# Optimization experiments

Measured on AMD Instinct MI355X. Metric: run time of the kernel, lower is better.

The kernel has to match this reference:

```python
import jax, jax.numpy as jnp
import numpy as np

N_NODES = 50000
E_TRAIN = 800000
E_POS = 200000
E_NEG = 200000
F_IN = 128


def gcn_conv(x, W, b, src, dst, n):
    """PyG-style GCNConv: add self-loops, symmetric deg^{-1/2} norm, linear, scatter-add."""
    loop = jnp.arange(n, dtype=src.dtype)
    s = jnp.concatenate([src, loop])  # [E+N]
    d = jnp.concatenate([dst, loop])
    deg = jax.ops.segment_sum(jnp.ones(d.shape, dtype=x.dtype), d, num_segments=n)
    dis = jax.lax.rsqrt(jnp.maximum(deg, 1.0))  # deg >= 1 due to self-loops
    norm = dis[s] * dis[d]  # [E+N]
    h = x @ W  # [N, out]
    msg = h[s] * norm[:, None]  # gather + per-edge scale
    return jax.ops.segment_sum(msg, d, num_segments=n) + b


def reference(x, train_pos_edge_index, pos_edge_index, neg_edge_index, W1, b1, W2, b2, W3, b3):
    src, dst = train_pos_edge_index[0], train_pos_edge_index[1]
    h = jax.nn.relu(gcn_conv(x, W1, b1, src, dst, N_NODES))
    h = jax.nn.relu(gcn_conv(h, W2, b2, src, dst, N_NODES))
    h = gcn_conv(h, W3, b3, src, dst, N_NODES)
    te = jnp.concatenate([pos_edge_index, neg_edge_index], axis=-1)  # [2, E_pos+E_neg]
    x_j = h[te[0]]
    x_i = h[te[1]]
    return jnp.einsum('ef,ef->e', x_i, x_j)


def setup_inputs() -> dict:
    key = jax.random.key(0)
    ks = jax.random.split(key, 10)
    glorot = lambda k, fi, fo: jax.random.normal(k, (fi, fo), dtype=jnp.float32) * np.float32(np.sqrt(2.0 / (fi + fo)))
    return {
        'x': jax.random.normal(ks[0], (N_NODES, F_IN), dtype=jnp.float32),
        'train_pos_edge_index': jax.random.randint(ks[1], (2, E_TRAIN), 0, N_NODES, dtype=jnp.int32),
        'pos_edge_index': jax.random.randint(ks[2], (2, E_POS), 0, N_NODES, dtype=jnp.int32),
        'neg_edge_index': jax.random.randint(ks[3], (2, E_NEG), 0, N_NODES, dtype=jnp.int32),
        'W1': glorot(ks[4], F_IN, 256), 'b1': jnp.zeros((256,), jnp.float32),
        'W2': glorot(ks[5], 256, 128), 'b2': jnp.zeros((128,), jnp.float32),
        'W3': glorot(ks[6], 128, 64), 'b3': jnp.zeros((64,), jnp.float32),
    }
```

## Files before the change

### kernel.cpp

```cpp
#include <hip/hip_runtime.h>
#include <math.h>

#define N_NODES 50000
#define E_TRAIN 800000
#define E_POS 200000
#define E_NEG 200000

#define NBUCK 196
#define BSTRIDE 5120


__device__ inline void split_bf16(float f, short& h, short& l) {
    unsigned u = __float_as_uint(f);
    h = (short)(u >> 16);
    float rem = f - __uint_as_float(u & 0xFFFF0000u);
    l = (short)(__float_as_uint(rem) >> 16);
}

__device__ inline unsigned short f2bf_rne(float f) {
    unsigned u = __float_as_uint(f);
    unsigned r = u + 0x7FFFu + ((u >> 16) & 1u);
    return (unsigned short)(r >> 16);
}

__device__ inline float bf2f(unsigned short h) {
    return __uint_as_float(((unsigned)h) << 16);
}


__global__ void partA_kernel(const int* __restrict__ src, const int* __restrict__ dst,
                             int* __restrict__ gcount, unsigned int* __restrict__ temp, int e) {
    __shared__ int hist[NBUCK];
    __shared__ int base[NBUCK];
    __shared__ int lcur[NBUCK];
    int tid = threadIdx.x;
    for (int i = tid; i < NBUCK; i += 256) hist[i] = 0;
    __syncthreads();
    int start = blockIdx.x * 4096;
    int stop = min(start + 4096, e);
    for (int i = start + tid; i < stop; i += 256)
        atomicAdd(&hist[dst[i] >> 8], 1);
    __syncthreads();
    for (int i = tid; i < NBUCK; i += 256) {
        base[i] = atomicAdd(&gcount[i], hist[i]);
        lcur[i] = 0;
    }
    __syncthreads();
    for (int i = start + tid; i < stop; i += 256) {
        int d = dst[i];
        int b = d >> 8;
        int off = atomicAdd(&lcur[b], 1);
        temp[(size_t)b * BSTRIDE + base[b] + off] = ((unsigned)src[i] << 8) | (unsigned)(d & 255);
    }
}

__global__ void scanb_kernel(const int* __restrict__ gcount, int* __restrict__ gbase) {
    __shared__ int s[256];
    int t = threadIdx.x;
    int v = (t < NBUCK) ? gcount[t] : 0;
    s[t] = v;
    __syncthreads();
    for (int d = 1; d < 256; d <<= 1) {
        int u = 0;
        if (t >= d) u = s[t - d];
        __syncthreads();
        if (t >= d) s[t] += u;
        __syncthreads();
    }
    if (t < NBUCK) gbase[t] = s[t] - v;
}


__global__ void partB_kernel(const unsigned int* __restrict__ temp,
                             const int* __restrict__ gcount, const int* __restrict__ gbase,
                             float* __restrict__ dis, int* __restrict__ offs, int* __restrict__ ends,
                             unsigned short* __restrict__ csr) {
    __shared__ int cnt[256];
    __shared__ int loc[256];
    __shared__ int cursor[256];
    int b = blockIdx.x;
    int t = threadIdx.x;
    int total = gcount[b];
    size_t tbase = (size_t)b * BSTRIDE;
    cnt[t] = 0;
    __syncthreads();
    for (int i = t; i < total; i += 256)
        atomicAdd(&cnt[temp[tbase + i] & 255], 1);
    __syncthreads();
    int c = cnt[t];
    loc[t] = c;
    __syncthreads();
    for (int d = 1; d < 256; d <<= 1) {
        int u = 0;
        if (t >= d) u = loc[t - d];
        __syncthreads();
        if (t >= d) loc[t] += u;
        __syncthreads();
    }
    int excl = loc[t] - c;
    int node = b * 256 + t;
    int gstart = gbase[b] + excl;
    if (node < N_NODES) {
        dis[node] = 1.0f / sqrtf((float)(c + 1));
        offs[node] = gstart;
        ends[node] = gstart + c;
    }
    cursor[t] = gstart;
    __syncthreads();
    for (int i = t; i < total; i += 256) {
        unsigned v = temp[tbase + i];
        int pos = atomicAdd(&cursor[v & 255], 1);
        csr[pos] = (unsigned short)(v >> 8);
    }
}

#define WTOT (128 * 256 + 256 * 128 + 128 * 64)

__global__ void prep_kernel(const float* __restrict__ W1, short* __restrict__ W1h, short* __restrict__ W1l,
                            const float* __restrict__ W2, short* __restrict__ W2h, short* __restrict__ W2l,
                            const float* __restrict__ W3, short* __restrict__ W3h, short* __restrict__ W3l,
                            const float* __restrict__ x, unsigned short* __restrict__ xb, int n4) {
    int i = blockIdx.x * blockDim.x + threadIdx.x;
    if (i < WTOT) {
        const float* W; short *Wh, *Wl; int K, N;
        if (i < 128 * 256) { W = W1; Wh = W1h; Wl = W1l; K = 128; N = 256; }
        else if (i < 128 * 256 + 256 * 128) { i -= 128 * 256; W = W2; Wh = W2h; Wl = W2l; K = 256; N = 128; }
        else { i -= 128 * 256 + 256 * 128; W = W3; Wh = W3h; Wl = W3l; K = 128; N = 64; }
        int k = i / N, n = i - k * N;
        short h, l;
        split_bf16(W[i], h, l);
        Wh[(size_t)n * K + k] = h;
        Wl[(size_t)n * K + k] = l;
    } else {
        int j = i - WTOT;
        if (j < n4) {
            float4 v = ((const float4*)x)[j];
            ushort4 o;
            o.x = f2bf_rne(v.x); o.y = f2bf_rne(v.y);
            o.z = f2bf_rne(v.z); o.w = f2bf_rne(v.w);
            ((ushort4*)xb)[j] = o;
        }
    }
}


typedef short bf16x8 __attribute__((ext_vector_type(8)));
typedef float f32x4 __attribute__((ext_vector_type(4)));

template<int BN, bool BR, bool OBF>
__global__ __launch_bounds__(512) void gemm_fulln_kernel(
        const float* __restrict__ A,
        const short* __restrict__ Bth, const short* __restrict__ Btl,
        const float* __restrict__ bias, float* __restrict__ C,
        unsigned short* __restrict__ Cb,
        int M, int K) {
    constexpr int NI = BN / 16;
    constexpr int BCH = BN * 4;
    constexpr int BP = (BCH + 511) / 512;
    constexpr size_t BSZ = (size_t)2 * BN * 40 * 2;
    constexpr size_t TSZ = (size_t)8 * 16 * 68 * 4;
    __shared__ __align__(16) char smem[BSZ > TSZ ? BSZ : TSZ];
    short* Bhi = (short*)smem;
    short* Blo = (short*)(smem + (size_t)BN * 40 * 2);
    float* tr  = (float*)smem;

    int tid = threadIdx.x;
    int lane = tid & 63;
    int wv = tid >> 6;
    int brow = blockIdx.x * 128;
    int m_lane = lane & 15;
    int kgrp = lane >> 4;

    int myrow = brow + wv * 16 + m_lane;
    if (myrow >= M) myrow = M - 1;
    const float* Ap = &A[(size_t)myrow * K + kgrp * 8];

    f32x4 acc[NI];
    #pragma unroll
    for (int i = 0; i < NI; i++) acc[i] = (f32x4){0.f, 0.f, 0.f, 0.f};

    int4 bhReg[BP], blReg[BP];
    float4 aN0, aN1, aC0, aC1;

    auto loadB = [&](int k0) {
        #pragma unroll
        for (int p = 0; p < BP; p++) {
            int idx = p * 512 + tid;
            if (idx < BCH) {
                int col = idx >> 2;
                int kc = idx & 3;
                size_t o = (size_t)col * K + k0 + kc * 8;
                bhReg[p] = *(const int4*)&Bth[o];
                blReg[p] = *(const int4*)&Btl[o];
            }
        }
    };
    auto loadA = [&](int k0) {
        aN0 = *(const float4*)&Ap[k0];
        aN1 = *(const float4*)&Ap[k0 + 4];
    };

    loadB(0); loadA(0);

    for (int k0 = 0; k0 < K; k0 += 32) {
        aC0 = aN0; aC1 = aN1;
        #pragma unroll
        for (int p = 0; p < BP; p++) {
            int idx = p * 512 + tid;
            if (idx < BCH) {
                int col = idx >> 2;
                int kc = idx & 3;
                *(int4*)&Bhi[col * 40 + kc * 8] = bhReg[p];
                *(int4*)&Blo[col * 40 + kc * 8] = blReg[p];
            }
        }
        __syncthreads();

        if (k0 + 32 < K) { loadB(k0 + 32); loadA(k0 + 32); }

        bf16x8 ah, al;
        {
            short h, l;
            split_bf16(aC0.x, h, l); ah[0] = h; al[0] = l;
            split_bf16(aC0.y, h, l); ah[1] = h; al[1] = l;
            split_bf16(aC0.z, h, l); ah[2] = h; al[2] = l;
            split_bf16(aC0.w, h, l); ah[3] = h; al[3] = l;
            split_bf16(aC1.x, h, l); ah[4] = h; al[4] = l;
            split_bf16(aC1.y, h, l); ah[5] = h; al[5] = l;
            split_bf16(aC1.z, h, l); ah[6] = h; al[6] = l;
            split_bf16(aC1.w, h, l); ah[7] = h; al[7] = l;
        }
        #pragma unroll
        for (int ni = 0; ni < NI; ni++) {
            int boff = (ni * 16 + m_lane) * 40 + kgrp * 8;
            bf16x8 bh = *(const bf16x8*)&Bhi[boff];
            bf16x8 bl = *(const bf16x8*)&Blo[boff];
            acc[ni] = __builtin_amdgcn_mfma_f32_16x16x32_bf16(ah, bh, acc[ni], 0, 0, 0);
            acc[ni] = __builtin_amdgcn_mfma_f32_16x16x32_bf16(al, bh, acc[ni], 0, 0, 0);
            acc[ni] = __builtin_amdgcn_mfma_f32_16x16x32_bf16(ah, bl, acc[ni], 0, 0, 0);
        }
        __syncthreads();
    }

    #pragma unroll
    for (int c = 0; c < NI / 4; c++) {
        #pragma unroll
        for (int q = 0; q < 4; q++) {
            int ni = c * 4 + q;
            float bb = 0.f;
            if (BR) bb = bias[ni * 16 + m_lane];
            #pragma unroll
            for (int reg = 0; reg < 4; reg++) {
                float v = acc[ni][reg];
                if (BR) v = fmaxf(v + bb, 0.f);
                tr[wv * 1088 + (kgrp * 4 + reg) * 68 + q * 16 + m_lane] = v;
            }
        }
        #pragma unroll
        for (int j = 0; j < 4; j++) {
            int r = (lane >> 4) + j * 4;
            int g = lane & 15;
            float4 v = *(const float4*)&tr[wv * 1088 + r * 68 + g * 4];
            int row = brow + wv * 16 + r;
            if (row < M) {
                if (OBF) {
                    ushort4 o;
                    o.x = f2bf_rne(v.x); o.y = f2bf_rne(v.y);
                    o.z = f2bf_rne(v.z); o.w = f2bf_rne(v.w);
                    *(ushort4*)&Cb[(size_t)row * BN + c * 64 + g * 4] = o;
                } else {
                    *(float4*)&C[(size_t)row * BN + c * 64 + g * 4] = v;
                }
            }
        }
    }
}


#define AGG_WAVES 12800
#define AGG_BLOCKS (AGG_WAVES / 4)

template<int F, bool RELU, bool BIAS>
__global__ void aggregate_bf16_kernel(const unsigned short* __restrict__ xb,
                                      float* __restrict__ out,
                                      const float* __restrict__ dis,
                                      const int* __restrict__ starts,
                                      const int* __restrict__ ends,
                                      const unsigned short* __restrict__ csr_src,
                                      const float* __restrict__ bias,
                                      int n) {
    int wid = (blockIdx.x * blockDim.x + threadIdx.x) >> 6;
    int lane = threadIdx.x & 63;
    constexpr int VPT = F / 64;

    for (int v = wid; v < n; v += AGG_WAVES) {
        float dv = dis[v];
        float acc[VPT];
        if constexpr (VPT == 2) {
            ushort2 sv = *(const ushort2*)&xb[(size_t)v * F + lane * 2];
            acc[0] = bf2f(sv.x) * dv * dv;
            acc[1] = bf2f(sv.y) * dv * dv;
        } else {
            acc[0] = bf2f(xb[(size_t)v * F + lane]) * dv * dv;
        }
        int s = starts[v], e = ends[v];
        int p = s;
        for (; p + 16 <= e; p += 16) {
            int u[16];
            #pragma unroll
            for (int q = 0; q < 16; q++) u[q] = csr_src[p + q];
            float w[16];
            #pragma unroll
            for (int q = 0; q < 16; q++) w[q] = dis[u[q]] * dv;
            if constexpr (VPT == 2) {
                ushort2 g[16];
                #pragma unroll
                for (int q = 0; q < 16; q++)
                    g[q] = *(const ushort2*)&xb[(size_t)u[q] * F + lane * 2];
                #pragma unroll
                for (int q = 0; q < 16; q++) {
                    acc[0] += bf2f(g[q].x) * w[q];
                    acc[1] += bf2f(g[q].y) * w[q];
                }
            } else {
                unsigned short g[16];
                #pragma unroll
                for (int q = 0; q < 16; q++)
                    g[q] = xb[(size_t)u[q] * F + lane];
                #pragma unroll
                for (int q = 0; q < 16; q++) acc[0] += bf2f(g[q]) * w[q];
            }
        }
        for (; p + 8 <= e; p += 8) {
            int u[8];
            #pragma unroll
            for (int q = 0; q < 8; q++) u[q] = csr_src[p + q];
            float w[8];
            #pragma unroll
            for (int q = 0; q < 8; q++) w[q] = dis[u[q]] * dv;
            if constexpr (VPT == 2) {
                ushort2 g[8];
                #pragma unroll
                for (int q = 0; q < 8; q++)
                    g[q] = *(const ushort2*)&xb[(size_t)u[q] * F + lane * 2];
                #pragma unroll
                for (int q = 0; q < 8; q++) {
                    acc[0] += bf2f(g[q].x) * w[q];
                    acc[1] += bf2f(g[q].y) * w[q];
                }
            } else {
                unsigned short g[8];
                #pragma unroll
                for (int q = 0; q < 8; q++)
                    g[q] = xb[(size_t)u[q] * F + lane];
                #pragma unroll
                for (int q = 0; q < 8; q++) acc[0] += bf2f(g[q]) * w[q];
            }
        }
        for (; p < e; p++) {
            int u = csr_src[p];
            float w = dis[u] * dv;
            if constexpr (VPT == 2) {
                ushort2 g = *(const ushort2*)&xb[(size_t)u * F + lane * 2];
                acc[0] += bf2f(g.x) * w;
                acc[1] += bf2f(g.y) * w;
            } else {
                acc[0] += bf2f(xb[(size_t)u * F + lane]) * w;
            }
        }
        float* o = &out[(size_t)v * F + lane * VPT];
        #pragma unroll
        for (int i = 0; i < VPT; i++) {
            float r = acc[i];
            if (BIAS) r += bias[lane * VPT + i];
            if (RELU) r = fmaxf(r, 0.f);
            o[i] = r;
        }
    }
}


__global__ void dot_kernel(const float* __restrict__ h,
                           const int* __restrict__ pos, const int* __restrict__ neg,
                           float* __restrict__ out) {
    int gw = (blockIdx.x * blockDim.x + threadIdx.x) >> 6;
    int lane = threadIdx.x & 63;
    int sub = lane >> 4;
    int pl = lane & 15;
    int e = gw * 4 + sub;
    if (e >= E_POS + E_NEG) return;
    int i0, i1;
    if (e < E_POS) { i0 = pos[e]; i1 = pos[E_POS + e]; }
    else { int t = e - E_POS; i0 = neg[t]; i1 = neg[E_NEG + t]; }
    float4 a = *(const float4*)&h[(size_t)i0 * 64 + pl * 4];
    float4 b = *(const float4*)&h[(size_t)i1 * 64 + pl * 4];
    float v = a.x * b.x + a.y * b.y + a.z * b.z + a.w * b.w;
    v += __shfl_xor(v, 1, 64);
    v += __shfl_xor(v, 2, 64);
    v += __shfl_xor(v, 4, 64);
    v += __shfl_xor(v, 8, 64);
    if (pl == 0) out[e] = v;
}


extern "C" void kernel_launch(void* const* d_in, const int* in_sizes, int n_in,
                              void* d_out, int out_size, void* d_ws, size_t ws_size,
                              hipStream_t stream) {
    const float* x  = (const float*)d_in[0];
    const int* tei  = (const int*)d_in[1];
    const int* pos  = (const int*)d_in[2];
    const int* neg  = (const int*)d_in[3];
    const float* W1 = (const float*)d_in[4];
    const float* b1 = (const float*)d_in[5];
    const float* W2 = (const float*)d_in[6];
    const float* b2 = (const float*)d_in[7];
    const float* W3 = (const float*)d_in[8];
    const float* b3 = (const float*)d_in[9];
    float* out = (float*)d_out;

    const int* src = tei;
    const int* dst = tei + E_TRAIN;

    char* ws = (char*)d_ws;
    size_t off = 0;
    auto alloc = [&](size_t bytes) -> void* {
        void* p = ws + off;
        off = (off + bytes + 255) & ~(size_t)255;
        return p;
    };
    unsigned short* xb   = (unsigned short*)alloc((size_t)N_NODES * 128 * 2);
    float* aggX          = (float*)alloc((size_t)N_NODES * 128 * 4);
    float* h1            = (float*)alloc((size_t)N_NODES * 256 * 4);
    unsigned short* xw2b = (unsigned short*)alloc((size_t)N_NODES * 128 * 2);
    float* h2            = (float*)alloc((size_t)N_NODES * 128 * 4);
    unsigned short* xw3b = (unsigned short*)alloc((size_t)N_NODES * 64 * 2);
    float* h3            = (float*)alloc((size_t)N_NODES * 64 * 4);
    float* dis  = (float*)alloc(N_NODES * 4);
    int* offs   = (int*)alloc(N_NODES * 4);
    int* ends   = (int*)alloc(N_NODES * 4);
    int* gcount = (int*)alloc(NBUCK * 4);
    int* gbase  = (int*)alloc(NBUCK * 4);
    unsigned int* temp  = (unsigned int*)alloc((size_t)NBUCK * BSTRIDE * 4);
    unsigned short* csr = (unsigned short*)alloc((size_t)E_TRAIN * 2);
    short* Wt1h = (short*)alloc((size_t)128 * 256 * 2);
    short* Wt1l = (short*)alloc((size_t)128 * 256 * 2);
    short* Wt2h = (short*)alloc((size_t)256 * 128 * 2);
    short* Wt2l = (short*)alloc((size_t)256 * 128 * 2);
    short* Wt3h = (short*)alloc((size_t)128 * 64 * 2);
    short* Wt3l = (short*)alloc((size_t)128 * 64 * 2);
    (void)ws_size; (void)n_in; (void)in_sizes; (void)out_size;

    hipMemsetAsync(gcount, 0, NBUCK * 4, stream);
    partA_kernel<<<(E_TRAIN + 4095) / 4096, 256, 0, stream>>>(src, dst, gcount, temp, E_TRAIN);
    scanb_kernel<<<1, 256, 0, stream>>>(gcount, gbase);
    partB_kernel<<<NBUCK, 256, 0, stream>>>(temp, gcount, gbase, dis, offs, ends, csr);

    const int n4 = N_NODES * 128 / 4;
    prep_kernel<<<(WTOT + n4 + 255) / 256, 256, 0, stream>>>(
        W1, Wt1h, Wt1l, W2, Wt2h, Wt2l, W3, Wt3h, Wt3l, x, xb, n4);

    const int GB = (N_NODES + 127) / 128;

    aggregate_bf16_kernel<128, false, false><<<AGG_BLOCKS, 256, 0, stream>>>(
        xb, aggX, dis, offs, ends, csr, nullptr, N_NODES);
    gemm_fulln_kernel<256, true, false><<<GB, 512, 0, stream>>>(
        aggX, Wt1h, Wt1l, b1, h1, nullptr, N_NODES, 128);

    gemm_fulln_kernel<128, false, true><<<GB, 512, 0, stream>>>(
        h1, Wt2h, Wt2l, nullptr, nullptr, xw2b, N_NODES, 256);
    aggregate_bf16_kernel<128, true, true><<<AGG_BLOCKS, 256, 0, stream>>>(
        xw2b, h2, dis, offs, ends, csr, b2, N_NODES);

    gemm_fulln_kernel<64, false, true><<<GB, 512, 0, stream>>>(
        h2, Wt3h, Wt3l, nullptr, nullptr, xw3b, N_NODES, 128);
    aggregate_bf16_kernel<64, false, true><<<AGG_BLOCKS, 256, 0, stream>>>(
        xw3b, h3, dis, offs, ends, csr, b3, N_NODES);

    const int DOT_WAVES = (E_POS + E_NEG + 3) / 4;
    dot_kernel<<<(DOT_WAVES + 3) / 4, 256, 0, stream>>>(h3, pos, neg, out);
}
```

Measured before the change: 330.5 us.

## Pad CSR rows to 16, precompute per-edge source norms, fuse partition with prep

Pads each node's CSR neighbor list to a multiple of 16, using fixed per-bucket strides so the global scan kernel is no longer needed. A new pass stores each edge's source deg^-1/2 in a separate array, with padding entries pointing at node 0 with weight zero. The aggregation loop can then use vector loads of indices and weights and drops its 8-wide and scalar tail loops. The partition and weight/x conversion kernels are merged into one launch. In exchange there is an extra kernel, more memory traffic for padded edges and the weight array, and wasted gathers on padding.

```diff
diff --git a/kernel.cpp b/kernel.cpp
--- a/kernel.cpp
+++ b/kernel.cpp
@@ -8,6 +8,8 @@
 
 #define NBUCK 196
 #define BSTRIDE 5120
+#define PSTRIDE 9216
+#define PARTA_BLOCKS 196
 
 
 __device__ inline void split_bf16(float f, short& h, short& l) {
@@ -27,52 +29,67 @@
     return __uint_as_float(((unsigned)h) << 16);
 }
 
-
-__global__ void partA_kernel(const int* __restrict__ src, const int* __restrict__ dst,
-                             int* __restrict__ gcount, unsigned int* __restrict__ temp, int e) {
+#define WTOT (128 * 256 + 256 * 128 + 128 * 64)
+
+
+__global__ void partA_prep_kernel(
+        const int* __restrict__ src, const int* __restrict__ dst,
+        int* __restrict__ gcount, unsigned int* __restrict__ temp, int e,
+        const float* __restrict__ W1, short* __restrict__ W1h, short* __restrict__ W1l,
+        const float* __restrict__ W2, short* __restrict__ W2h, short* __restrict__ W2l,
+        const float* __restrict__ W3, short* __restrict__ W3h, short* __restrict__ W3l,
+        const float* __restrict__ x, unsigned short* __restrict__ xb, int n4) {
     __shared__ int hist[NBUCK];
     __shared__ int base[NBUCK];
     __shared__ int lcur[NBUCK];
     int tid = threadIdx.x;
-    for (int i = tid; i < NBUCK; i += 256) hist[i] = 0;
-    __syncthreads();
-    int start = blockIdx.x * 4096;
-    int stop = min(start + 4096, e);
-    for (int i = start + tid; i < stop; i += 256)
-        atomicAdd(&hist[dst[i] >> 8], 1);
-    __syncthreads();
-    for (int i = tid; i < NBUCK; i += 256) {
-        base[i] = atomicAdd(&gcount[i], hist[i]);
-        lcur[i] = 0;
-    }
-    __syncthreads();
-    for (int i = start + tid; i < stop; i += 256) {
-        int d = dst[i];
-        int b = d >> 8;
-        int off = atomicAdd(&lcur[b], 1);
-        temp[(size_t)b * BSTRIDE + base[b] + off] = ((unsigned)src[i] << 8) | (unsigned)(d & 255);
-    }
-}
-
-__global__ void scanb_kernel(const int* __restrict__ gcount, int* __restrict__ gbase) {
-    __shared__ int s[256];
-    int t = threadIdx.x;
-    int v = (t < NBUCK) ? gcount[t] : 0;
-    s[t] = v;
-    __syncthreads();
-    for (int d = 1; d < 256; d <<= 1) {
-        int u = 0;
-        if (t >= d) u = s[t - d];
-        __syncthreads();
-        if (t >= d) s[t] += u;
-        __syncthreads();
-    }
-    if (t < NBUCK) gbase[t] = s[t] - v;
+    if (blockIdx.x < PARTA_BLOCKS) {
+        for (int i = tid; i < NBUCK; i += 256) hist[i] = 0;
+        __syncthreads();
+        int start = blockIdx.x * 4096;
+        int stop = min(start + 4096, e);
+        for (int i = start + tid; i < stop; i += 256)
+            atomicAdd(&hist[dst[i] >> 8], 1);
+        __syncthreads();
+        for (int i = tid; i < NBUCK; i += 256) {
+            base[i] = atomicAdd(&gcount[i], hist[i]);
+            lcur[i] = 0;
+        }
+        __syncthreads();
+        for (int i = start + tid; i < stop; i += 256) {
+            int d = dst[i];
+            int b = d >> 8;
+            int off = atomicAdd(&lcur[b], 1);
+            temp[(size_t)b * BSTRIDE + base[b] + off] = ((unsigned)src[i] << 8) | (unsigned)(d & 255);
+        }
+    } else {
+        int i = (blockIdx.x - PARTA_BLOCKS) * 256 + tid;
+        if (i < WTOT) {
+            const float* W; short *Wh, *Wl; int K, N;
+            if (i < 128 * 256) { W = W1; Wh = W1h; Wl = W1l; K = 128; N = 256; }
+            else if (i < 128 * 256 + 256 * 128) { i -= 128 * 256; W = W2; Wh = W2h; Wl = W2l; K = 256; N = 128; }
+            else { i -= 128 * 256 + 256 * 128; W = W3; Wh = W3h; Wl = W3l; K = 128; N = 64; }
+            int k = i / N, n = i - k * N;
+            short h, l;
+            split_bf16(W[i], h, l);
+            Wh[(size_t)n * K + k] = h;
+            Wl[(size_t)n * K + k] = l;
+        } else {
+            int j = i - WTOT;
+            if (j < n4) {
+                float4 v = ((const float4*)x)[j];
+                ushort4 o;
+                o.x = f2bf_rne(v.x); o.y = f2bf_rne(v.y);
+                o.z = f2bf_rne(v.z); o.w = f2bf_rne(v.w);
+                ((ushort4*)xb)[j] = o;
+            }
+        }
+    }
 }
 
 
 __global__ void partB_kernel(const unsigned int* __restrict__ temp,
-                             const int* __restrict__ gcount, const int* __restrict__ gbase,
+                             const int* __restrict__ gcount,
                              float* __restrict__ dis, int* __restrict__ offs, int* __restrict__ ends,
                              unsigned short* __restrict__ csr) {
     __shared__ int cnt[256];
@@ -88,7 +105,8 @@
         atomicAdd(&cnt[temp[tbase + i] & 255], 1);
     __syncthreads();
     int c = cnt[t];
-    loc[t] = c;
+    int pc = (c + 15) & ~15;
+    loc[t] = pc;
     __syncthreads();
     for (int d = 1; d < 256; d <<= 1) {
         int u = 0;
@@ -97,13 +115,13 @@
         if (t >= d) loc[t] += u;
         __syncthreads();
     }
-    int excl = loc[t] - c;
+    int excl = loc[t] - pc;
     int node = b * 256 + t;
-    int gstart = gbase[b] + excl;
+    int gstart = b * PSTRIDE + excl;
     if (node < N_NODES) {
         dis[node] = 1.0f / sqrtf((float)(c + 1));
         offs[node] = gstart;
-        ends[node] = gstart + c;
+        ends[node] = gstart + pc;
     }
     cursor[t] = gstart;
     __syncthreads();
@@ -112,34 +130,19 @@
         int pos = atomicAdd(&cursor[v & 255], 1);
         csr[pos] = (unsigned short)(v >> 8);
     }
-}
-
-#define WTOT (128 * 256 + 256 * 128 + 128 * 64)
-
-__global__ void prep_kernel(const float* __restrict__ W1, short* __restrict__ W1h, short* __restrict__ W1l,
-                            const float* __restrict__ W2, short* __restrict__ W2h, short* __restrict__ W2l,
-                            const float* __restrict__ W3, short* __restrict__ W3h, short* __restrict__ W3l,
-                            const float* __restrict__ x, unsigned short* __restrict__ xb, int n4) {
+    __syncthreads();
+    for (int j = c; j < pc; j++)
+        csr[gstart + j] = 0xFFFFu;
+}
+
+__global__ void wdis_kernel(unsigned short* __restrict__ csr,
+                            const float* __restrict__ dis,
+                            float* __restrict__ wdis, int n) {
     int i = blockIdx.x * blockDim.x + threadIdx.x;
-    if (i < WTOT) {
-        const float* W; short *Wh, *Wl; int K, N;
-        if (i < 128 * 256) { W = W1; Wh = W1h; Wl = W1l; K = 128; N = 256; }
-        else if (i < 128 * 256 + 256 * 128) { i -= 128 * 256; W = W2; Wh = W2h; Wl = W2l; K = 256; N = 128; }
-        else { i -= 128 * 256 + 256 * 128; W = W3; Wh = W3h; Wl = W3l; K = 128; N = 64; }
-        int k = i / N, n = i - k * N;
-        short h, l;
-        split_bf16(W[i], h, l);
-        Wh[(size_t)n * K + k] = h;
-        Wl[(size_t)n * K + k] = l;
-    } else {
-        int j = i - WTOT;
-        if (j < n4) {
-            float4 v = ((const float4*)x)[j];
-            ushort4 o;
-            o.x = f2bf_rne(v.x); o.y = f2bf_rne(v.y);
-            o.z = f2bf_rne(v.z); o.w = f2bf_rne(v.w);
-            ((ushort4*)xb)[j] = o;
-        }
+    if (i < n) {
+        unsigned short s = csr[i];
+        if (s == 0xFFFFu) { csr[i] = 0; wdis[i] = 0.f; }
+        else wdis[i] = dis[s];
     }
 }
 
@@ -287,6 +290,7 @@
                                       const int* __restrict__ starts,
                                       const int* __restrict__ ends,
                                       const unsigned short* __restrict__ csr_src,
+                                      const float* __restrict__ wdis,
                                       const float* __restrict__ bias,
                                       int n) {
     int wid = (blockIdx.x * blockDim.x + threadIdx.x) >> 6;
@@ -303,15 +307,29 @@
         } else {
             acc[0] = bf2f(xb[(size_t)v * F + lane]) * dv * dv;
         }
-        int s = starts[v], e = ends[v];
-        int p = s;
-        for (; p + 16 <= e; p += 16) {
+        int s = __builtin_amdgcn_readfirstlane(starts[v]);
+        int e = __builtin_amdgcn_readfirstlane(ends[v]);
+        for (int p = s; p < e; p += 16) {
+            int4 c0 = *(const int4*)&csr_src[p];
+            int4 c1 = *(const int4*)&csr_src[p + 8];
+            float4 w0 = *(const float4*)&wdis[p];
+            float4 w1 = *(const float4*)&wdis[p + 4];
+            float4 w2 = *(const float4*)&wdis[p + 8];
+            float4 w3 = *(const float4*)&wdis[p + 12];
             int u[16];
-            #pragma unroll
-            for (int q = 0; q < 16; q++) u[q] = csr_src[p + q];
+            u[0] = (unsigned)c0.x & 0xFFFF; u[1] = (unsigned)c0.x >> 16;
+            u[2] = (unsigned)c0.y & 0xFFFF; u[3] = (unsigned)c0.y >> 16;
+            u[4] = (unsigned)c0.z & 0xFFFF; u[5] = (unsigned)c0.z >> 16;
+            u[6] = (unsigned)c0.w & 0xFFFF; u[7] = (unsigned)c0.w >> 16;
+            u[8] = (unsigned)c1.x & 0xFFFF; u[9] = (unsigned)c1.x >> 16;
+            u[10] = (unsigned)c1.y & 0xFFFF; u[11] = (unsigned)c1.y >> 16;
+            u[12] = (unsigned)c1.z & 0xFFFF; u[13] = (unsigned)c1.z >> 16;
+            u[14] = (unsigned)c1.w & 0xFFFF; u[15] = (unsigned)c1.w >> 16;
             float w[16];
-            #pragma unroll
-            for (int q = 0; q < 16; q++) w[q] = dis[u[q]] * dv;
+            w[0] = w0.x * dv; w[1] = w0.y * dv; w[2] = w0.z * dv; w[3] = w0.w * dv;
+            w[4] = w1.x * dv; w[5] = w1.y * dv; w[6] = w1.z * dv; w[7] = w1.w * dv;
+            w[8] = w2.x * dv; w[9] = w2.y * dv; w[10] = w2.z * dv; w[11] = w2.w * dv;
+            w[12] = w3.x * dv; w[13] = w3.y * dv; w[14] = w3.z * dv; w[15] = w3.w * dv;
             if constexpr (VPT == 2) {
                 ushort2 g[16];
                 #pragma unroll
@@ -329,43 +347,6 @@
                     g[q] = xb[(size_t)u[q] * F + lane];
                 #pragma unroll
                 for (int q = 0; q < 16; q++) acc[0] += bf2f(g[q]) * w[q];
-            }
-        }
-        for (; p + 8 <= e; p += 8) {
-            int u[8];
-            #pragma unroll
-            for (int q = 0; q < 8; q++) u[q] = csr_src[p + q];
-            float w[8];
-            #pragma unroll
-            for (int q = 0; q < 8; q++) w[q] = dis[u[q]] * dv;
-            if constexpr (VPT == 2) {
-                ushort2 g[8];
-                #pragma unroll
-                for (int q = 0; q < 8; q++)
-                    g[q] = *(const ushort2*)&xb[(size_t)u[q] * F + lane * 2];
-                #pragma unroll
-                for (int q = 0; q < 8; q++) {
-                    acc[0] += bf2f(g[q].x) * w[q];
-                    acc[1] += bf2f(g[q].y) * w[q];
-                }
-            } else {
-                unsigned short g[8];
-                #pragma unroll
-                for (int q = 0; q < 8; q++)
-                    g[q] = xb[(size_t)u[q] * F + lane];
-                #pragma unroll
-                for (int q = 0; q < 8; q++) acc[0] += bf2f(g[q]) * w[q];
-            }
-        }
-        for (; p < e; p++) {
-            int u = csr_src[p];
-            float w = dis[u] * dv;
-            if constexpr (VPT == 2) {
-                ushort2 g = *(const ushort2*)&xb[(size_t)u * F + lane * 2];
-                acc[0] += bf2f(g.x) * w;
-                acc[1] += bf2f(g.y) * w;
-            } else {
-                acc[0] += bf2f(xb[(size_t)u * F + lane]) * w;
             }
         }
         float* o = &out[(size_t)v * F + lane * VPT];
@@ -439,9 +420,9 @@
     int* offs   = (int*)alloc(N_NODES * 4);
     int* ends   = (int*)alloc(N_NODES * 4);
     int* gcount = (int*)alloc(NBUCK * 4);
-    int* gbase  = (int*)alloc(NBUCK * 4);
     unsigned int* temp  = (unsigned int*)alloc((size_t)NBUCK * BSTRIDE * 4);
-    unsigned short* csr = (unsigned short*)alloc((size_t)E_TRAIN * 2);
+    unsigned short* csr = (unsigned short*)alloc((size_t)NBUCK * PSTRIDE * 2);
+    float* wdis         = (float*)alloc((size_t)NBUCK * PSTRIDE * 4);
     short* Wt1h = (short*)alloc((size_t)128 * 256 * 2);
     short* Wt1l = (short*)alloc((size_t)128 * 256 * 2);
     short* Wt2h = (short*)alloc((size_t)256 * 128 * 2);
@@ -450,31 +431,37 @@
     short* Wt3l = (short*)alloc((size_t)128 * 64 * 2);
     (void)ws_size; (void)n_in; (void)in_sizes; (void)out_size;
 
+    const int n4 = N_NODES * 128 / 4;
+
     hipMemsetAsync(gcount, 0, NBUCK * 4, stream);
-    partA_kernel<<<(E_TRAIN + 4095) / 4096, 256, 0, stream>>>(src, dst, gcount, temp, E_TRAIN);
-    scanb_kernel<<<1, 256, 0, stream>>>(gcount, gbase);
-    partB_kernel<<<NBUCK, 256, 0, stream>>>(temp, gcount, gbase, dis, offs, ends, csr);
-
-    const int n4 = N_NODES * 128 / 4;
-    prep_kernel<<<(WTOT + n4 + 255) / 256, 256, 0, stream>>>(
-        W1, Wt1h, Wt1l, W2, Wt2h, Wt2l, W3, Wt3h, Wt3l, x, xb, n4);
+    {
+        int prep_blocks = (WTOT + n4 + 255) / 256;
+        partA_prep_kernel<<<PARTA_BLOCKS + prep_blocks, 256, 0, stream>>>(
+            src, dst, gcount, temp, E_TRAIN,
+            W1, Wt1h, Wt1l, W2, Wt2h, Wt2l, W3, Wt3h, Wt3l, x, xb, n4);
+    }
+    partB_kernel<<<NBUCK, 256, 0, stream>>>(temp, gcount, dis, offs, ends, csr);
+    {
+        int ncsr = NBUCK * PSTRIDE;
+        wdis_kernel<<<(ncsr + 255) / 256, 256, 0, stream>>>(csr, dis, wdis, ncsr);
+    }
 
     const int GB = (N_NODES + 127) / 128;
 
     aggregate_bf16_kernel<128, false, false><<<AGG_BLOCKS, 256, 0, stream>>>(
-        xb, aggX, dis, offs, ends, csr, nullptr, N_NODES);
+        xb, aggX, dis, offs, ends, csr, wdis, nullptr, N_NODES);
     gemm_fulln_kernel<256, true, false><<<GB, 512, 0, stream>>>(
         aggX, Wt1h, Wt1l, b1, h1, nullptr, N_NODES, 128);
 
     gemm_fulln_kernel<128, false, true><<<GB, 512, 0, stream>>>(
         h1, Wt2h, Wt2l, nullptr, nullptr, xw2b, N_NODES, 256);
     aggregate_bf16_kernel<128, true, true><<<AGG_BLOCKS, 256, 0, stream>>>(
-        xw2b, h2, dis, offs, ends, csr, b2, N_NODES);
+        xw2b, h2, dis, offs, ends, csr, wdis, b2, N_NODES);
 
     gemm_fulln_kernel<64, false, true><<<GB, 512, 0, stream>>>(
         h2, Wt3h, Wt3l, nullptr, nullptr, xw3b, N_NODES, 128);
     aggregate_bf16_kernel<64, false, true><<<AGG_BLOCKS, 256, 0, stream>>>(
-        xw3b, h3, dis, offs, ends, csr, b3, N_NODES);
+        xw3b, h3, dis, offs, ends, csr, wdis, b3, N_NODES);
 
     const int DOT_WAVES = (E_POS + E_NEG + 3) / 4;
     dot_kernel<<<(DOT_WAVES + 3) / 4, 256, 0, stream>>>(h3, pos, neg, out);
```

Result: faster. 295.6 us (-10.6%).
